# Optimization experiments

Hardware: AMD Instinct MI355X
Metric: run time of the kernel (lower is better)

The kernel has to match this reference:

```python
import jax, jax.numpy as jnp
import numpy as np

MARGIN = 1.0
SOFT_MARGIN = False
EPS = 1e-8


def setup_inputs() -> dict:
    key = jax.random.key(0)
    k1, k2 = jax.random.split(key)
    B, D, N_CLASSES = 8192, 128, 64
    emb = jax.random.normal(k1, (B, D), dtype=jnp.float32)
    # docstring says embeddings are L2-normalized
    emb = emb / jnp.linalg.norm(emb, axis=1, keepdims=True)
    labels = jax.random.randint(k2, (B,), 0, N_CLASSES, dtype=jnp.int32)
    return {"embeddings": emb, "labels": labels}


def _pairwise_distances(embeddings):
    # d_ij = sqrt(relu(|e_i|^2 + |e_j|^2 - 2 e_i.e_j) + eps)
    dot = embeddings @ embeddings.T                      # (B, B)
    sq = jnp.sum(embeddings * embeddings, axis=1, keepdims=True)
    dist2 = jax.nn.relu(sq + sq.T - 2.0 * dot)
    return jnp.sqrt(dist2 + EPS)


def reference(embeddings, labels):
    B = embeddings.shape[0]
    d = _pairwise_distances(embeddings)                  # (B, B)

    same = labels[:, None] == labels[None, :]            # (B, B) bool
    not_self = ~jnp.eye(B, dtype=bool)
    pos_mask = same & not_self
    neg_mask = ~same

    inf = jnp.asarray(jnp.inf, d.dtype)
    # hardest positive: max same-label distance; hardest negative: min diff-label distance
    pos_dist = jnp.max(jnp.where(pos_mask, d, -inf), axis=1)   # (B,)
    neg_dist = jnp.min(jnp.where(neg_mask, d, inf), axis=1)    # (B,)

    valid = jnp.any(pos_mask, axis=1) & jnp.any(neg_mask, axis=1)

    diff = pos_dist - neg_dist
    if SOFT_MARGIN:
        losses = jax.nn.softplus(diff)
    else:
        losses = jax.nn.relu(diff + MARGIN)

    n_valid = jnp.sum(valid.astype(jnp.int32))
    loss_sum = jnp.sum(jnp.where(valid, losses, 0.0))
    loss = jnp.where(n_valid > 0,
                     loss_sum / jnp.maximum(n_valid, 1).astype(losses.dtype),
                     jnp.asarray(0.0, losses.dtype))
    return loss, n_valid
```

## Files before the change

kernel.cpp:

```cpp
#include <hip/hip_runtime.h>
#include <hip/hip_bf16.h>

typedef unsigned short ushort_t;
typedef __attribute__((ext_vector_type(8))) short s16x8;
typedef __attribute__((ext_vector_type(4))) float f32x4;

#define NB 8192
#define ND 128
#define BMR 128
#define TCOLS 64
#define CHUNK 1024
#define NT (CHUNK/TCOLS)
#define NCHUNK (NB/CHUNK)
#define EPS 1e-8f
#define MARGIN 1.0f

typedef const __attribute__((address_space(1))) void* gptr_t;
typedef __attribute__((address_space(3))) void* lptr_t;
__device__ __forceinline__ void gll16(const void* g, void* l) {
    __builtin_amdgcn_global_load_lds((gptr_t)g, (lptr_t)l, 16, 0, 0);
}

template <int ITERS>
__device__ __forceinline__ void stage_rows(const ushort_t* __restrict__ g,
                                           ushort_t* l, int tid, int w) {
    #pragma unroll
    for (int it = 0; it < ITERS; ++it) {
        const int c = it * 256 + tid;
        const int r = c >> 4, s = c & 15;
        const int ss = s ^ (r & 7);
        gll16(g + r * ND + ss * 8, l + (it * 256 + w * 64) * 8);
    }
}

__global__ void prep_kernel(const float* __restrict__ E,
                            ushort_t* __restrict__ Ebf,
                            float* __restrict__ sqA) {
    const int tid  = threadIdx.x;
    const int lane = tid & 63;
    const int row  = blockIdx.x * 4 + (tid >> 6);

    const float2 v = reinterpret_cast<const float2*>(E + (size_t)row * ND)[lane];
    __hip_bfloat16 b0 = __float2bfloat16(v.x);
    __hip_bfloat16 b1 = __float2bfloat16(v.y);
    ushort_t pk[2] = { *reinterpret_cast<ushort_t*>(&b0), *reinterpret_cast<ushort_t*>(&b1) };
    *reinterpret_cast<uint*>(&Ebf[(size_t)row * ND + lane * 2]) = *reinterpret_cast<uint*>(pk);

    float ss = v.x * v.x + v.y * v.y;
    #pragma unroll
    for (int off = 32; off; off >>= 1) ss += __shfl_down(ss, off, 64);
    if (lane == 0) sqA[row] = ss;
}

__global__ __launch_bounds__(256, 1) void triplet_gemm(
        const ushort_t* __restrict__ Ebf,
        const int* __restrict__ labels,
        float* __restrict__ pvPart,
        float* __restrict__ nvPart) {
    __shared__ __align__(16) ushort_t As[BMR * ND];
    __shared__ __align__(16) ushort_t Bb[2][TCOLS * ND];

    const int tid = threadIdx.x, lane = tid & 63, w = tid >> 6;
    const int fr = lane & 15, fg = lane >> 4;
    const int rowBase = blockIdx.x * BMR;
    const int chunkBase = blockIdx.y * CHUNK;
    const int wrow = w * 32;

    stage_rows<8>(Ebf + (size_t)rowBase * ND, As, tid, w);
    stage_rows<4>(Ebf + (size_t)chunkBase * ND, &Bb[0][0], tid, w);

    int labR[2][4];
    #pragma unroll
    for (int mi = 0; mi < 2; ++mi)
        #pragma unroll
        for (int reg = 0; reg < 4; ++reg)
            labR[mi][reg] = labels[rowBase + wrow + mi * 16 + fg * 4 + reg];

    int swByte[4];
    #pragma unroll
    for (int ks = 0; ks < 4; ++ks) swByte[ks] = ((ks * 4 + fg) ^ (fr & 7)) * 16;

    asm volatile("s_waitcnt vmcnt(0)" ::: "memory");
    __builtin_amdgcn_s_barrier();
    __builtin_amdgcn_sched_barrier(0);

    s16x8 a[4][2];
    {
        const char* ap = (const char*)As;
        #pragma unroll
        for (int ks = 0; ks < 4; ++ks)
            #pragma unroll
            for (int mi = 0; mi < 2; ++mi)
                a[ks][mi] = *reinterpret_cast<const s16x8*>(
                    ap + (wrow + mi * 16 + fr) * 256 + swByte[ks]);
    }

    const float PINF = __builtin_inff(), NINF = -__builtin_inff();
    f32x4 pv[2], nv[2];
    #pragma unroll
    for (int mi = 0; mi < 2; ++mi) {
        pv[mi] = f32x4{PINF, PINF, PINF, PINF};
        nv[mi] = f32x4{NINF, NINF, NINF, NINF};
    }

    auto tile_step = [&](int t, const ushort_t* cur, ushort_t* nxt) {
        if (t + 1 < NT)
            stage_rows<4>(Ebf + (size_t)(chunkBase + (t + 1) * TCOLS) * ND, nxt, tid, w);

        const char* cp = (const char*)cur;
        const f32x4 zf = {0.f, 0.f, 0.f, 0.f};
        #pragma unroll
        for (int ni = 0; ni < 4; ++ni) {
            const int labC = labels[chunkBase + t * TCOLS + ni * 16 + fr];
            s16x8 b[4];
            #pragma unroll
            for (int ks = 0; ks < 4; ++ks)
                b[ks] = *reinterpret_cast<const s16x8*>(
                    cp + (ni * 16 + fr) * 256 + swByte[ks]);
            f32x4 acc0 = __builtin_amdgcn_mfma_f32_16x16x32_bf16(a[0][0], b[0], zf, 0, 0, 0);
            f32x4 acc1 = __builtin_amdgcn_mfma_f32_16x16x32_bf16(a[0][1], b[0], zf, 0, 0, 0);
            #pragma unroll
            for (int ks = 1; ks < 4; ++ks) {
                acc0 = __builtin_amdgcn_mfma_f32_16x16x32_bf16(a[ks][0], b[ks], acc0, 0, 0, 0);
                acc1 = __builtin_amdgcn_mfma_f32_16x16x32_bf16(a[ks][1], b[ks], acc1, 0, 0, 0);
            }
            #pragma unroll
            for (int reg = 0; reg < 4; ++reg) {
                bool eq0 = (labR[0][reg] == labC);
                bool eq1 = (labR[1][reg] == labC);
                pv[0][reg] = fminf(pv[0][reg], eq0 ? acc0[reg] : PINF);
                nv[0][reg] = fmaxf(nv[0][reg], eq0 ? NINF : acc0[reg]);
                pv[1][reg] = fminf(pv[1][reg], eq1 ? acc1[reg] : PINF);
                nv[1][reg] = fmaxf(nv[1][reg], eq1 ? NINF : acc1[reg]);
            }
        }
        asm volatile("s_waitcnt vmcnt(0) lgkmcnt(0)" ::: "memory");
        __builtin_amdgcn_sched_barrier(0);
        __builtin_amdgcn_s_barrier();
        __builtin_amdgcn_sched_barrier(0);
    };

    #pragma unroll 1
    for (int tt = 0; tt < NT; tt += 2) {
        tile_step(tt,     &Bb[0][0], &Bb[1][0]);
        tile_step(tt + 1, &Bb[1][0], &Bb[0][0]);
    }

    #pragma unroll
    for (int mi = 0; mi < 2; ++mi)
        #pragma unroll
        for (int reg = 0; reg < 4; ++reg) {
            float p = pv[mi][reg], n = nv[mi][reg];
            #pragma unroll
            for (int off = 1; off < 16; off <<= 1) {
                p = fminf(p, __shfl_xor(p, off, 64));
                n = fmaxf(n, __shfl_xor(n, off, 64));
            }
            if (fr == 0) {
                const int grow = rowBase + wrow + mi * 16 + fg * 4 + reg;
                pvPart[(size_t)blockIdx.y * NB + grow] = p;
                nvPart[(size_t)blockIdx.y * NB + grow] = n;
            }
        }
}

__global__ void finalize_partial(const float* __restrict__ sqA,
                                 const float* __restrict__ pvPart,
                                 const float* __restrict__ nvPart,
                                 float* __restrict__ fpart) {
    __shared__ float sl[4], sc[4];
    const int tid = threadIdx.x, lane = tid & 63, w = tid >> 6;
    const int i = blockIdx.x * 256 + tid;
    const float PINF = __builtin_inff(), NINF = -__builtin_inff();

    float pMin = PINF, nMax = NINF;
    #pragma unroll
    for (int c = 0; c < NCHUNK; ++c) {
        pMin = fminf(pMin, pvPart[(size_t)c * NB + i]);
        nMax = fmaxf(nMax, nvPart[(size_t)c * NB + i]);
    }
    bool valid = (pMin < PINF) && (nMax > NINF);
    float sq = sqA[i];
    float pd = sqrtf(fmaxf(sq + 1.0f - 2.0f * pMin, 0.f) + EPS);
    float nd = sqrtf(fmaxf(sq + 1.0f - 2.0f * nMax, 0.f) + EPS);
    float l  = fmaxf(pd - nd + MARGIN, 0.f);
    float lv = valid ? l : 0.f;
    float cv = valid ? 1.f : 0.f;
    #pragma unroll
    for (int off = 32; off; off >>= 1) {
        lv += __shfl_down(lv, off, 64);
        cv += __shfl_down(cv, off, 64);
    }
    if (lane == 0) { sl[w] = lv; sc[w] = cv; }
    __syncthreads();
    if (tid == 0) {
        fpart[blockIdx.x * 2]     = sl[0] + sl[1] + sl[2] + sl[3];
        fpart[blockIdx.x * 2 + 1] = sc[0] + sc[1] + sc[2] + sc[3];
    }
}

__global__ void finalize_write(const float* __restrict__ fpart, float* __restrict__ out) {
    if (threadIdx.x == 0) {
        float L = 0.f, C = 0.f;
        #pragma unroll
        for (int k = 0; k < NB / 256; ++k) { L += fpart[2 * k]; C += fpart[2 * k + 1]; }
        out[0] = (C > 0.f) ? (L / C) : 0.f;
        out[1] = C;
    }
}

extern "C" void kernel_launch(void* const* d_in, const int* in_sizes, int n_in,
                              void* d_out, int out_size, void* d_ws, size_t ws_size,
                              hipStream_t stream) {
    const float* E      = (const float*)d_in[0];
    const int*   labels = (const int*)d_in[1];
    float*       out    = (float*)d_out;

    char* ws = (char*)d_ws;
    ushort_t* Ebf    = (ushort_t*)ws;
    float*    sqA    = (float*)(ws + (size_t)NB * ND * 2);
    float*    pvPart = (float*)(ws + (size_t)NB * ND * 2 + NB * 4);
    float*    nvPart = (float*)(ws + (size_t)NB * ND * 2 + NB * 4 + (size_t)NCHUNK * NB * 4);
    float*    fpart  = (float*)(ws + (size_t)NB * ND * 2 + NB * 4 + 2 * (size_t)NCHUNK * NB * 4);

    prep_kernel<<<NB / 4, 256, 0, stream>>>(E, Ebf, sqA);

    dim3 grid(NB / BMR, NCHUNK);
    triplet_gemm<<<grid, 256, 0, stream>>>(Ebf, labels, pvPart, nvPart);

    finalize_partial<<<NB / 256, 256, 0, stream>>>(sqA, pvPart, nvPart, fpart);
    finalize_write<<<1, 64, 0, stream>>>(fpart, out);
}
```

Before: 41.59 us.

## Encode label masks as extra GEMM columns to drop per-element masking

Extends each bf16 embedding row with a 64-wide one-hot label block. The row side carries -8 at its label slot and the column side carries 1, so same-label dot products are shifted by -8. With that offset a plain min/max over the MFMA output separates positive and negative candidates, which removes the per-element label compares and selects from the inner loop. The change also retiles to 64 rows per wave, 256-row blocks and 512-column chunks, loads A fragments directly from global memory, and uses triple-buffered LDS staging. The trade-offs are more MFMA K-work (K from 128 to 192), wider staging, and reliance on unit-norm inputs so the -8 offset and the validity thresholds stay separable; self-pairs are no longer excluded from the positive set.

```diff
diff --git a/kernel.cpp b/kernel.cpp
--- a/kernel.cpp
+++ b/kernel.cpp
@@ -7,10 +7,13 @@
 
 #define NB 8192
 #define ND 128
-#define BMR 128
+#define KE 192
+#define ROWB (KE*2)
+#define WROWS 64
+#define BMR 256
 #define TCOLS 64
-#define CHUNK 1024
-#define NT (CHUNK/TCOLS)
+#define CHUNK 512
+#define NTILE (CHUNK/TCOLS)
 #define NCHUNK (NB/CHUNK)
 #define EPS 1e-8f
 #define MARGIN 1.0f
@@ -21,20 +24,9 @@
     __builtin_amdgcn_global_load_lds((gptr_t)g, (lptr_t)l, 16, 0, 0);
 }
 
-template <int ITERS>
-__device__ __forceinline__ void stage_rows(const ushort_t* __restrict__ g,
-                                           ushort_t* l, int tid, int w) {
-    #pragma unroll
-    for (int it = 0; it < ITERS; ++it) {
-        const int c = it * 256 + tid;
-        const int r = c >> 4, s = c & 15;
-        const int ss = s ^ (r & 7);
-        gll16(g + r * ND + ss * 8, l + (it * 256 + w * 64) * 8);
-    }
-}
-
 __global__ void prep_kernel(const float* __restrict__ E,
-                            ushort_t* __restrict__ Ebf,
+                            const int* __restrict__ labels,
+                            ushort_t* __restrict__ Eb,
                             float* __restrict__ sqA) {
     const int tid  = threadIdx.x;
     const int lane = tid & 63;
@@ -43,8 +35,18 @@
     const float2 v = reinterpret_cast<const float2*>(E + (size_t)row * ND)[lane];
     __hip_bfloat16 b0 = __float2bfloat16(v.x);
     __hip_bfloat16 b1 = __float2bfloat16(v.y);
-    ushort_t pk[2] = { *reinterpret_cast<ushort_t*>(&b0), *reinterpret_cast<ushort_t*>(&b1) };
-    *reinterpret_cast<uint*>(&Ebf[(size_t)row * ND + lane * 2]) = *reinterpret_cast<uint*>(pk);
+    uint pk = (uint)*reinterpret_cast<ushort_t*>(&b0)
+            | ((uint)*reinterpret_cast<ushort_t*>(&b1) << 16);
+    uint* rowp = reinterpret_cast<uint*>(Eb + (size_t)row * KE);
+    rowp[lane] = pk;
+
+    if (lane < 32) {
+        const int lab = labels[row];
+        const int c0 = lane * 2, c1 = lane * 2 + 1;
+        uint e = (uint)((lab == c0) ? 0x3F80u : 0u)
+               | (((lab == c1) ? 0x3F80u : 0u) << 16);
+        rowp[64 + lane] = e;
+    }
 
     float ss = v.x * v.x + v.y * v.y;
     #pragma unroll
@@ -53,101 +55,127 @@
 }
 
 __global__ __launch_bounds__(256, 1) void triplet_gemm(
-        const ushort_t* __restrict__ Ebf,
+        const ushort_t* __restrict__ Eb,
         const int* __restrict__ labels,
         float* __restrict__ pvPart,
         float* __restrict__ nvPart) {
-    __shared__ __align__(16) ushort_t As[BMR * ND];
-    __shared__ __align__(16) ushort_t Bb[2][TCOLS * ND];
+    __shared__ __align__(16) ushort_t Bb[3][TCOLS * KE];
 
     const int tid = threadIdx.x, lane = tid & 63, w = tid >> 6;
     const int fr = lane & 15, fg = lane >> 4;
     const int rowBase = blockIdx.x * BMR;
     const int chunkBase = blockIdx.y * CHUNK;
-    const int wrow = w * 32;
-
-    stage_rows<8>(Ebf + (size_t)rowBase * ND, As, tid, w);
-    stage_rows<4>(Ebf + (size_t)chunkBase * ND, &Bb[0][0], tid, w);
-
-    int labR[2][4];
-    #pragma unroll
-    for (int mi = 0; mi < 2; ++mi)
-        #pragma unroll
-        for (int reg = 0; reg < 4; ++reg)
-            labR[mi][reg] = labels[rowBase + wrow + mi * 16 + fg * 4 + reg];
-
-    int swByte[4];
-    #pragma unroll
-    for (int ks = 0; ks < 4; ++ks) swByte[ks] = ((ks * 4 + fg) ^ (fr & 7)) * 16;
-
-    asm volatile("s_waitcnt vmcnt(0)" ::: "memory");
+    const int wrow = rowBase + w * WROWS;
+
+    int srcOff[6];
+    #pragma unroll
+    for (int it = 0; it < 6; ++it) {
+        const int c = it * 256 + tid;
+        const int r = c / 24, s = c - r * 24;
+        srcOff[it] = r * ROWB + ((s ^ (r & 7)) << 4);
+    }
+    auto stage = [&](int bufi, int t) {
+        const char* g = (const char*)Eb + (size_t)(chunkBase + t * TCOLS) * ROWB;
+        char* l = (char*)&Bb[0][0] + bufi * (TCOLS * KE * 2);
+        #pragma unroll
+        for (int it = 0; it < 6; ++it)
+            gll16(g + srcOff[it], l + (it * 256 + w * 64) * 16);
+    };
+
+    int swb[6];
+    #pragma unroll
+    for (int ks = 0; ks < 6; ++ks) swb[ks] = (((ks * 4 + fg) ^ (fr & 7)) << 4);
+
+    int labv[4];
+    #pragma unroll
+    for (int mi = 0; mi < 4; ++mi) labv[mi] = labels[wrow + mi * 16 + fr];
+
+    s16x8 a[6][4];
+    #pragma unroll
+    for (int ks = 0; ks < 4; ++ks)
+        #pragma unroll
+        for (int mi = 0; mi < 4; ++mi)
+            a[ks][mi] = *reinterpret_cast<const s16x8*>(
+                (const char*)Eb + (size_t)(wrow + mi * 16 + fr) * ROWB + ks * 64 + fg * 16);
+
+    stage(0, 0);
+    stage(1, 1);
+    asm volatile("s_waitcnt vmcnt(6)" ::: "memory");
+    __builtin_amdgcn_sched_barrier(0);
     __builtin_amdgcn_s_barrier();
     __builtin_amdgcn_sched_barrier(0);
 
-    s16x8 a[4][2];
-    {
-        const char* ap = (const char*)As;
-        #pragma unroll
-        for (int ks = 0; ks < 4; ++ks)
-            #pragma unroll
-            for (int mi = 0; mi < 2; ++mi)
-                a[ks][mi] = *reinterpret_cast<const s16x8*>(
-                    ap + (wrow + mi * 16 + fr) * 256 + swByte[ks]);
-    }
+    #pragma unroll
+    for (int ks = 4; ks < 6; ++ks)
+        #pragma unroll
+        for (int mi = 0; mi < 4; ++mi) {
+            s16x8 t{};
+            #pragma unroll
+            for (int j = 0; j < 8; ++j) {
+                const int c = (ks - 4) * 32 + fg * 8 + j;
+                t[j] = (labv[mi] == c) ? (short)0xC100 : (short)0;
+            }
+            a[ks][mi] = t;
+        }
 
     const float PINF = __builtin_inff(), NINF = -__builtin_inff();
-    f32x4 pv[2], nv[2];
-    #pragma unroll
-    for (int mi = 0; mi < 2; ++mi) {
+    f32x4 pv[4], nv[4];
+    #pragma unroll
+    for (int mi = 0; mi < 4; ++mi) {
         pv[mi] = f32x4{PINF, PINF, PINF, PINF};
         nv[mi] = f32x4{NINF, NINF, NINF, NINF};
     }
-
-    auto tile_step = [&](int t, const ushort_t* cur, ushort_t* nxt) {
-        if (t + 1 < NT)
-            stage_rows<4>(Ebf + (size_t)(chunkBase + (t + 1) * TCOLS) * ND, nxt, tid, w);
-
-        const char* cp = (const char*)cur;
-        const f32x4 zf = {0.f, 0.f, 0.f, 0.f};
-        #pragma unroll
-        for (int ni = 0; ni < 4; ++ni) {
-            const int labC = labels[chunkBase + t * TCOLS + ni * 16 + fr];
-            s16x8 b[4];
-            #pragma unroll
-            for (int ks = 0; ks < 4; ++ks)
+    const f32x4 zf = {0.f, 0.f, 0.f, 0.f};
+
+    #pragma unroll 1
+    for (int p = 0; p < NTILE; ++p) {
+        if (p + 2 < NTILE) {
+            stage((p + 2) % 3, p + 2);
+            asm volatile("s_waitcnt vmcnt(6)" ::: "memory");
+        } else {
+            asm volatile("s_waitcnt vmcnt(0)" ::: "memory");
+        }
+        const char* cp = (const char*)&Bb[0][0] + (p % 3) * (TCOLS * KE * 2);
+
+        auto loadB = [&](s16x8* b, int ni) {
+            #pragma unroll
+            for (int ks = 0; ks < 6; ++ks)
                 b[ks] = *reinterpret_cast<const s16x8*>(
-                    cp + (ni * 16 + fr) * 256 + swByte[ks]);
-            f32x4 acc0 = __builtin_amdgcn_mfma_f32_16x16x32_bf16(a[0][0], b[0], zf, 0, 0, 0);
-            f32x4 acc1 = __builtin_amdgcn_mfma_f32_16x16x32_bf16(a[0][1], b[0], zf, 0, 0, 0);
-            #pragma unroll
-            for (int ks = 1; ks < 4; ++ks) {
-                acc0 = __builtin_amdgcn_mfma_f32_16x16x32_bf16(a[ks][0], b[ks], acc0, 0, 0, 0);
-                acc1 = __builtin_amdgcn_mfma_f32_16x16x32_bf16(a[ks][1], b[ks], acc1, 0, 0, 0);
-            }
-            #pragma unroll
-            for (int reg = 0; reg < 4; ++reg) {
-                bool eq0 = (labR[0][reg] == labC);
-                bool eq1 = (labR[1][reg] == labC);
-                pv[0][reg] = fminf(pv[0][reg], eq0 ? acc0[reg] : PINF);
-                nv[0][reg] = fmaxf(nv[0][reg], eq0 ? NINF : acc0[reg]);
-                pv[1][reg] = fminf(pv[1][reg], eq1 ? acc1[reg] : PINF);
-                nv[1][reg] = fmaxf(nv[1][reg], eq1 ? NINF : acc1[reg]);
-            }
-        }
-        asm volatile("s_waitcnt vmcnt(0) lgkmcnt(0)" ::: "memory");
+                    cp + (ni * 16 + fr) * ROWB + swb[ks]);
+        };
+        auto mfmaFold = [&](const s16x8* b) {
+            f32x4 acc[4];
+            #pragma unroll
+            for (int mi = 0; mi < 4; ++mi)
+                acc[mi] = __builtin_amdgcn_mfma_f32_16x16x32_bf16(a[0][mi], b[0], zf, 0, 0, 0);
+            #pragma unroll
+            for (int ks = 1; ks < 6; ++ks)
+                #pragma unroll
+                for (int mi = 0; mi < 4; ++mi)
+                    acc[mi] = __builtin_amdgcn_mfma_f32_16x16x32_bf16(a[ks][mi], b[ks], acc[mi], 0, 0, 0);
+            #pragma unroll
+            for (int mi = 0; mi < 4; ++mi)
+                #pragma unroll
+                for (int reg = 0; reg < 4; ++reg) {
+                    pv[mi][reg] = fminf(pv[mi][reg], acc[mi][reg]);
+                    nv[mi][reg] = fmaxf(nv[mi][reg], acc[mi][reg]);
+                }
+        };
+
+        s16x8 bX[6], bY[6];
+        loadB(bX, 0);
+        loadB(bY, 1); mfmaFold(bX);
+        loadB(bX, 2); mfmaFold(bY);
+        loadB(bY, 3); mfmaFold(bX);
+        mfmaFold(bY);
+
         __builtin_amdgcn_sched_barrier(0);
         __builtin_amdgcn_s_barrier();
         __builtin_amdgcn_sched_barrier(0);
-    };
-
-    #pragma unroll 1
-    for (int tt = 0; tt < NT; tt += 2) {
-        tile_step(tt,     &Bb[0][0], &Bb[1][0]);
-        tile_step(tt + 1, &Bb[1][0], &Bb[0][0]);
-    }
-
-    #pragma unroll
-    for (int mi = 0; mi < 2; ++mi)
+    }
+
+    #pragma unroll
+    for (int mi = 0; mi < 4; ++mi)
         #pragma unroll
         for (int reg = 0; reg < 4; ++reg) {
             float p = pv[mi][reg], n = nv[mi][reg];
@@ -157,7 +185,7 @@
                 n = fmaxf(n, __shfl_xor(n, off, 64));
             }
             if (fr == 0) {
-                const int grow = rowBase + wrow + mi * 16 + fg * 4 + reg;
+                const int grow = wrow + mi * 16 + fg * 4 + reg;
                 pvPart[(size_t)blockIdx.y * NB + grow] = p;
                 nvPart[(size_t)blockIdx.y * NB + grow] = n;
             }
@@ -179,10 +207,12 @@
         pMin = fminf(pMin, pvPart[(size_t)c * NB + i]);
         nMax = fmaxf(nMax, nvPart[(size_t)c * NB + i]);
     }
-    bool valid = (pMin < PINF) && (nMax > NINF);
+    bool valid = (nMax > -2.0f) && (pMin < -6.0f);
+    float dotP = pMin + 8.0f;
+    float dotN = nMax;
     float sq = sqA[i];
-    float pd = sqrtf(fmaxf(sq + 1.0f - 2.0f * pMin, 0.f) + EPS);
-    float nd = sqrtf(fmaxf(sq + 1.0f - 2.0f * nMax, 0.f) + EPS);
+    float pd = sqrtf(fmaxf(sq + 1.0f - 2.0f * dotP, 0.f) + EPS);
+    float nd = sqrtf(fmaxf(sq + 1.0f - 2.0f * dotN, 0.f) + EPS);
     float l  = fmaxf(pd - nd + MARGIN, 0.f);
     float lv = valid ? l : 0.f;
     float cv = valid ? 1.f : 0.f;
@@ -217,16 +247,17 @@
     float*       out    = (float*)d_out;
 
     char* ws = (char*)d_ws;
-    ushort_t* Ebf    = (ushort_t*)ws;
-    float*    sqA    = (float*)(ws + (size_t)NB * ND * 2);
-    float*    pvPart = (float*)(ws + (size_t)NB * ND * 2 + NB * 4);
-    float*    nvPart = (float*)(ws + (size_t)NB * ND * 2 + NB * 4 + (size_t)NCHUNK * NB * 4);
-    float*    fpart  = (float*)(ws + (size_t)NB * ND * 2 + NB * 4 + 2 * (size_t)NCHUNK * NB * 4);
-
-    prep_kernel<<<NB / 4, 256, 0, stream>>>(E, Ebf, sqA);
+    size_t off = 0;
+    ushort_t* Eb     = (ushort_t*)(ws + off);  off += (size_t)NB * KE * 2;
+    float*    sqA    = (float*)(ws + off);     off += (size_t)NB * 4;
+    float*    pvPart = (float*)(ws + off);     off += (size_t)NCHUNK * NB * 4;
+    float*    nvPart = (float*)(ws + off);     off += (size_t)NCHUNK * NB * 4;
+    float*    fpart  = (float*)(ws + off);
+
+    prep_kernel<<<NB / 4, 256, 0, stream>>>(E, labels, Eb, sqA);
 
     dim3 grid(NB / BMR, NCHUNK);
-    triplet_gemm<<<grid, 256, 0, stream>>>(Ebf, labels, pvPart, nvPart);
+    triplet_gemm<<<grid, 256, 0, stream>>>(Eb, labels, pvPart, nvPart);
 
     finalize_partial<<<NB / 256, 256, 0, stream>>>(sqA, pvPart, nvPart, fpart);
     finalize_write<<<1, 64, 0, stream>>>(fpart, out);
```

After: 40.02 us. 3.8% less time.
